# Kernel tuning notes

Measured on AMD Instinct MI355X. Metric: run time of the kernel, lower is better.

The kernel has to match this reference:

```python
import jax, jax.numpy as jnp
import numpy as np
from jax import lax

B, C, H, W, T = 1, 32, 256, 256, 10
Q = 0.2  # dropout prob; keep prob = 0.8


def conv2d(x, w, b=None, pad=0):
    out = lax.conv_general_dilated(x, w, (1, 1), [(pad, pad), (pad, pad)],
                                   dimension_numbers=('NCHW', 'OIHW', 'NCHW'))
    if b is not None:
        out = out + b[None, :, None, None]
    return out


def lrelu(v):
    return jnp.where(v > 0, v, 0.2 * v)


def setup_inputs() -> dict:
    key = jax.random.key(0)
    ks = iter(jax.random.split(key, 80))
    def rn(shape, s=0.05):
        return jax.random.normal(next(ks), shape, jnp.float32) * s
    d = {}
    d['F_1'] = jax.random.normal(next(ks), (B, C, H, W), jnp.float32)
    d['ms'] = jax.random.normal(next(ks), (B, 4, H, W), jnp.float32)
    d['pan'] = jax.random.normal(next(ks), (B, C, H, W), jnp.float32)
    d['masks_u'] = jax.random.uniform(next(ks), (T, 2 * C), jnp.float32)
    # UncertaintyEstimation params
    d['ue_conv_w'] = rn((2 * C, C, 3, 3)); d['ue_conv_b'] = rn((2 * C,), 0.01)
    d['ue_out_w'] = rn((4, 2 * C, 1, 1)); d['ue_out_b'] = rn((4,), 0.01)
    d['ue_aue_w'] = rn((4, 2 * C, 3, 3)); d['ue_aue_b'] = rn((4,), 0.01)
    # UAFM 1x1 convs
    d['conv1_w'] = rn((C, C, 1, 1)); d['conv1_b'] = rn((C,), 0.01)
    d['conv2_w'] = rn((C, C, 1, 1)); d['conv2_b'] = rn((C,), 0.01)
    # two UAConvs (condition_channels=4, channels_in=2C, channels_out=C, k=3)
    for i in (1, 2):
        d[f'spa{i}_w0'] = rn((9, 4, 3, 3)); d[f'spa{i}_b0'] = rn((9,), 0.01)
        d[f'spa{i}_w1'] = rn((9, 9, 1, 1)); d[f'spa{i}_b1'] = rn((9,), 0.01)
        d[f'spa{i}_w2'] = rn((9, 9, 1, 1)); d[f'spa{i}_b2'] = rn((9,), 0.01)
        d[f'spe{i}_w0'] = rn((2 * C, 4, 1, 1)); d[f'spe{i}_b0'] = rn((2 * C,), 0.01)
        d[f'spe{i}_w1'] = rn((2 * C, 2 * C, 1, 1)); d[f'spe{i}_b1'] = rn((2 * C,), 0.01)
        d[f'spe{i}_w2'] = rn((2 * C, 2 * C, 1, 1)); d[f'spe{i}_b2'] = rn((2 * C,), 0.01)
        d[f'ua{i}_w'] = rn((C, 2 * C, 3, 3))
    return d


def uaconv(x, U, sw0, sb0, sw1, sb1, sw2, sb2, pw0, pb0, pw1, pb1, pw2, pb2, Wk):
    # content-adaptive conv: per-pixel spatial (k*k) and spectral (n) attention
    b, n, h, w = x.shape
    a = jax.nn.relu(conv2d(U, sw0, sb0, 1))
    a = jax.nn.relu(conv2d(a, sw1, sb1, 0))
    spat = jax.nn.sigmoid(conv2d(a, sw2, sb2, 0))          # [B, 9, H, W]
    s = jax.nn.relu(conv2d(U, pw0, pb0, 0))
    s = jax.nn.relu(conv2d(s, pw1, pb1, 0))
    spec = jax.nn.sigmoid(conv2d(s, pw2, pb2, 0))          # [B, n, H, W]
    # unfold: patches channel order (c, kh, kw), matching F.unfold
    patches = lax.conv_general_dilated_patches(x, (3, 3), (1, 1), [(1, 1), (1, 1)])
    patches = patches.reshape(b, n, 9, h, w)               # [B, n, 9, H, W]
    rw = patches * spec[:, :, None] * spat[:, None]        # reweight
    Wr = Wk.reshape(Wk.shape[0], n, 9)                     # [m, n, 9]
    return jnp.einsum('bnkhw,mnk->bmhw', rw, Wr)           # fold(k=1) == reshape


def reference(F_1, ms, pan, masks_u,
              ue_conv_w, ue_conv_b, ue_out_w, ue_out_b, ue_aue_w, ue_aue_b,
              conv1_w, conv1_b, conv2_w, conv2_b,
              spa1_w0, spa1_b0, spa1_w1, spa1_b1, spa1_w2, spa1_b2,
              spe1_w0, spe1_b0, spe1_w1, spe1_b1, spe1_w2, spe1_b2, ua1_w,
              spa2_w0, spa2_b0, spa2_w1, spa2_b1, spa2_w2, spa2_b2,
              spe2_w0, spe2_b0, spe2_w1, spe2_b1, spe2_w2, spe2_b2, ua2_w):
    # --- UncertaintyEstimation ---
    x = conv2d(F_1, ue_conv_w, ue_conv_b, 1)               # [B, 2C, H, W]
    mask = (masks_u < (1.0 - Q)).astype(x.dtype)           # [T, 2C] Bernoulli(0.8)
    w4 = ue_out_w[:, :, 0, 0]                              # 1x1 conv as matmul
    # T masked passes, vectorized: xs [T, B, 4, H, W]
    xs = jnp.tanh(jnp.einsum('tc,oc,bchw->tbohw', mask, w4, x)
                  + ue_out_b[None, None, :, None, None]) + ms[None]
    EU = jnp.var(xs, axis=0, ddof=1)                       # unbiased over T
    mean = jnp.mean(xs, axis=0)
    AU = jax.nn.sigmoid(conv2d(x, ue_aue_w, ue_aue_b, 1))
    # --- UAFM ---
    y1 = uaconv(jnp.concatenate([F_1, pan], axis=1), EU,
                spa1_w0, spa1_b0, spa1_w1, spa1_b1, spa1_w2, spa1_b2,
                spe1_w0, spe1_b0, spe1_w1, spe1_b1, spe1_w2, spe1_b2, ua1_w)
    F_2 = lrelu(conv2d(y1, conv1_w, conv1_b, 0))
    y2 = uaconv(jnp.concatenate([F_1, F_2], axis=1), 1.0 - EU,
                spa2_w0, spa2_b0, spa2_w1, spa2_b1, spa2_w2, spa2_b2,
                spe2_w0, spe2_b0, spe2_w1, spe2_b1, spe2_w2, spe2_b2, ua2_w)
    F_out = lrelu(conv2d(y2, conv2_w, conv2_b, 0))
    return (AU, EU, mean, F_out)
```

## Files before the change

kernel.cpp:

```cpp
#include <hip/hip_runtime.h>
#include <hip/hip_bf16.h>
#include <math.h>
#include <string.h>

#define P 65536
#define HH 256
#define WW 256

typedef __attribute__((ext_vector_type(8))) short bf16x8;
typedef __attribute__((ext_vector_type(4))) float f32x4;

__device__ __forceinline__ float fast_sigmoid(float v) {
    return 1.f / (1.f + __expf(-v));
}
__device__ __forceinline__ float fast_tanh(float a) {
    a = fminf(fmaxf(a, -10.f), 10.f);
    float t = __expf(2.f * a);
    return (t - 1.f) / (t + 1.f);
}
__device__ __forceinline__ ushort f2bf(float f) {
    unsigned u = __float_as_uint(f);
    unsigned r = (u + 0x7fffu + ((u >> 16) & 1u)) >> 16;
    return (ushort)r;
}
__device__ __forceinline__ unsigned pack_bf2(float a, float b) {
    __hip_bfloat162 h = __float22bfloat162_rn(make_float2(a, b));
    unsigned u;
    memcpy(&u, &h, 4);
    return u;
}

__global__ __launch_bounds__(256) void setup_k(
        const float* __restrict__ F1, const float* __restrict__ pan,
        ushort* __restrict__ xbf, ushort* __restrict__ panbf,
        const float* __restrict__ ue_w, const float* __restrict__ aue_w,
        const float* __restrict__ ua1, const float* __restrict__ ua2,
        const float* __restrict__ s1w1, const float* __restrict__ s1w2,
        const float* __restrict__ s2w1, const float* __restrict__ s2w2,
        const float* __restrict__ cw1, const float* __restrict__ cw2,
        const float* __restrict__ masks_u, const float* __restrict__ w4,
        float* __restrict__ W, ushort* __restrict__ wub) {
    const int b = blockIdx.x;
    if (b < 512) {
        int idx = b * 256 + threadIdx.x;
        const float* src = (idx < P) ? F1 : pan;
        ushort* dst = (idx < P) ? xbf : panbf;
        int p = idx & (P - 1);
        unsigned pk[16];
        #pragma unroll
        for (int c = 0; c < 16; ++c) {
            float a = src[(2 * c) * P + p];
            float bb = src[(2 * c + 1) * P + p];
            pk[c] = (unsigned)f2bf(a) | ((unsigned)f2bf(bb) << 16);
        }
        uint4* d4 = (uint4*)(dst + (size_t)p * 32);
        #pragma unroll
        for (int q = 0; q < 4; ++q)
            d4[q] = make_uint4(pk[4 * q], pk[4 * q + 1], pk[4 * q + 2], pk[4 * q + 3]);
        return;
    }
    int i = (b - 512) * 256 + threadIdx.x;
    if (i < 2304) {
        int ci = i / 36, r = i % 36, k = r >> 2, co = r & 3;
        W[i] = aue_w[co * 576 + ci * 9 + k];
    } else if (i < 18688) {
    } else if (i < 21248) {
        int j = i - 18688;
        int t = j >> 8, o = (j >> 6) & 3, c = j & 63;
        W[i] = (masks_u[t * 64 + c] < 0.8f) ? w4[o * 64 + c] : 0.f;
    } else if (i < 39680) {
        int j = i - 21248;
        int ct = j / 4608, r1 = j % 4608;
        int kp = r1 / 512, r2 = r1 % 512;
        int n = r2 >> 5, ci = r2 & 31;
        wub[j] = f2bf(ue_w[(ct * 16 + n) * 288 + ci * 9 + kp]);
    } else if (i < 58112) {
        int j = i - 39680;
        int mo = j / 576, K = j % 576, k = K >> 6, n = K & 63;
        float s = 0.f;
        for (int m = 0; m < 32; ++m)
            s += cw1[mo * 32 + m] * ua1[m * 576 + n * 9 + k];
        wub[18432 + j] = f2bf(s);
    } else if (i < 76544) {
        int j = i - 58112;
        int mo = j / 576, K = j % 576, k = K >> 6, n = K & 63;
        float s = 0.f;
        for (int m = 0; m < 32; ++m)
            s += cw2[mo * 32 + m] * ua2[m * 576 + n * 9 + k];
        wub[36864 + j] = f2bf(s);
    } else if (i < 92928) {
        int j = i - 76544;
        int mat = j >> 12;
        int r = j & 4095;
        int ct = r >> 10, kk = (r >> 9) & 1, n = (r >> 5) & 15, c = r & 31;
        const float* src = (mat == 0) ? s1w1 : (mat == 1) ? s1w2
                         : (mat == 2) ? s2w1 : s2w2;
        wub[55296 + j] = f2bf(src[(ct * 16 + n) * 64 + kk * 32 + c]);
    }
}

__global__ __launch_bounds__(256) void conv_ue_mfma(
        const ushort* __restrict__ xbf, const ushort* __restrict__ wbfu,
        const float* __restrict__ bias, ushort* __restrict__ xnh) {
    __shared__ float tls[4][272];
    const int tid  = threadIdx.x;
    const int lane = tid & 63;
    const int wv   = __builtin_amdgcn_readfirstlane(tid >> 6);
    const int lrow = lane & 15;
    const int kg   = lane >> 4;

    bf16x8 zf;
    #pragma unroll
    for (int z = 0; z < 8; ++z) zf[z] = 0;

    bf16x8 Bf[9];
    const ushort* wb = wbfu + wv * 4608;
    #pragma unroll
    for (int kp = 0; kp < 9; ++kp)
        Bf[kp] = *(const bf16x8*)(wb + kp * 512 + lrow * 32 + kg * 8);

    const float bco = bias[wv * 16 + lrow];
    float* tw = tls[wv];

    for (int si = 0; si < 4; ++si) {
        const int s   = blockIdx.x * 4 + si;
        const int row = s >> 4;
        const int cb  = (s & 15) << 4;
        const int pb  = s << 4;
        f32x4 acc = {bco, bco, bco, bco};
        #pragma unroll
        for (int dh = -1; dh <= 1; ++dh) {
            if ((unsigned)(row + dh) >= 256u) continue;
            #pragma unroll
            for (int dw = -1; dw <= 1; ++dw) {
                const bool kill = (dw == -1 && cb == 0 && lrow == 0) ||
                                  (dw == 1 && cb == 240 && lrow == 15);
                const int apx = kill ? pb : (pb + dh * 256 + dw + lrow);
                bf16x8 Af = *(const bf16x8*)(xbf + (size_t)apx * 32 + kg * 8);
                if (kill) Af = zf;
                acc = __builtin_amdgcn_mfma_f32_16x16x32_bf16(
                          Af, Bf[(dh + 1) * 3 + (dw + 1)], acc, 0, 0, 0);
            }
        }
        #pragma unroll
        for (int j = 0; j < 4; ++j)
            tw[(kg * 4 + j) * 17 + lrow] = acc[j];
        asm volatile("s_waitcnt lgkmcnt(0)" ::: "memory");
        {
            const float* rp = tw + lrow * 17;
            unsigned o[8];
            #pragma unroll
            for (int q = 0; q < 8; ++q)
                o[q] = pack_bf2(rp[2 * q], rp[2 * q + 1]);
            ushort* dst = xnh + (size_t)(pb + lrow) * 64 + wv * 16;
            *(uint4*)dst       = make_uint4(o[0], o[1], o[2], o[3]);
            *(uint4*)(dst + 8) = make_uint4(o[4], o[5], o[6], o[7]);
        }
        asm volatile("s_waitcnt lgkmcnt(0)" ::: "memory");
    }
}

__global__ __launch_bounds__(256) void head_k(
        const ushort* __restrict__ xnh, const float* __restrict__ aue_wt,
        const float* __restrict__ aue_b, const float* __restrict__ mw,
        const float* __restrict__ b4, const float* __restrict__ msin,
        float* __restrict__ AU, float* __restrict__ EU, float* __restrict__ MEAN) {
    __shared__ float cs[64][65];
    __shared__ float pr[4][4][64];
    const int tid = threadIdx.x;
    const int pxg = tid & 63;
    const int g   = __builtin_amdgcn_readfirstlane(tid >> 6);
    const int p   = blockIdx.x * 64 + pxg;
    const int h = p >> 8, x0 = p & 255;
    const int cib = g * 16;

    float pa[4] = {0.f, 0.f, 0.f, 0.f};
    float cv[16];
    #pragma unroll
    for (int k = 0; k < 9; ++k) {
        const int dh = k / 3 - 1, dw = k % 3 - 1;
        if ((unsigned)(h + dh) >= 256u) continue;
        const bool kill = (dw == -1 && x0 == 0) || (dw == 1 && x0 == 255);
        const int pxe = kill ? p : (p + dh * 256 + dw);
        const ushort* sp = xnh + (size_t)pxe * 64 + cib;
        uint4 ra = *(const uint4*)sp;
        uint4 rb = *(const uint4*)(sp + 8);
        unsigned rr[8] = {ra.x, ra.y, ra.z, ra.w, rb.x, rb.y, rb.z, rb.w};
        if (kill) {
            #pragma unroll
            for (int q = 0; q < 8; ++q) rr[q] = 0;
        }
        float f[16];
        #pragma unroll
        for (int q = 0; q < 8; ++q) {
            f[2 * q]     = __uint_as_float(rr[q] << 16);
            f[2 * q + 1] = __uint_as_float(rr[q] & 0xffff0000u);
        }
        if (k == 4) {
            #pragma unroll
            for (int ci = 0; ci < 16; ++ci) cv[ci] = f[ci];
        }
        #pragma unroll
        for (int ci = 0; ci < 16; ++ci) {
            const float* wp = aue_wt + (cib + ci) * 36 + k * 4;
            #pragma unroll
            for (int co = 0; co < 4; ++co)
                pa[co] = fmaf(f[ci], wp[co], pa[co]);
        }
    }
    #pragma unroll
    for (int co = 0; co < 4; ++co) pr[co][g][pxg] = pa[co];
    #pragma unroll
    for (int ci = 0; ci < 16; ++ci) cs[pxg][cib + ci] = cv[ci];
    __syncthreads();

    {
        float s = aue_b[g] + pr[g][0][pxg] + pr[g][1][pxg]
                           + pr[g][2][pxg] + pr[g][3][pxg];
        AU[g * P + p] = fast_sigmoid(s);
    }

    float xv[64];
    #pragma unroll
    for (int c = 0; c < 64; ++c) xv[c] = cs[pxg][c];
    float msv = msin[g * P + p];
    float bo  = b4[g];
    float vals[10];
    float s = 0.f;
    #pragma unroll
    for (int t = 0; t < 10; ++t) {
        float a = bo;
        const float* mwp = mw + t * 256 + g * 64;
        #pragma unroll
        for (int c = 0; c < 64; ++c) a = fmaf(mwp[c], xv[c], a);
        float v = fast_tanh(a) + msv;
        vals[t] = v;
        s += v;
    }
    float m = s * 0.1f;
    MEAN[g * P + p] = m;
    float var = 0.f;
    #pragma unroll
    for (int t = 0; t < 10; ++t) { float d = vals[t] - m; var = fmaf(d, d, var); }
    EU[g * P + p] = var * (1.0f / 9.0f);
}

template<int OUTMODE>
__global__ __launch_bounds__(256) void ua_fused_k(
        const float* __restrict__ U, int flip,
        const float* __restrict__ aw0, const float* __restrict__ ab0,
        const float* __restrict__ aw1, const float* __restrict__ ab1,
        const float* __restrict__ aw2, const float* __restrict__ ab2,
        const float* __restrict__ pw0, const float* __restrict__ pb0,
        const float* __restrict__ pb1, const float* __restrict__ pb2,
        const ushort* __restrict__ wspe,
        const ushort* __restrict__ xa, const ushort* __restrict__ xb,
        const ushort* __restrict__ w2bf, const float* __restrict__ cb,
        float* __restrict__ outf, ushort* __restrict__ outh) {
    __shared__ __align__(16) ushort ping[64 * 72];
    __shared__ __align__(16) ushort pong[64 * 72];
    __shared__ float spat_l[9][64];
    const int tid = threadIdx.x;
    const int pxg = tid & 63;
    const int g   = __builtin_amdgcn_readfirstlane(tid >> 6);
    const int cib = g * 16;
    const int p   = blockIdx.x * 64 + pxg;
    const int h = p >> 8, x0 = p & 255;
    const int lane = tid & 63;
    const int lrow = lane & 15;
    const int kg   = lane >> 4;

    bf16x8 Wf[2][4][2];
    #pragma unroll
    for (int ly = 0; ly < 2; ++ly)
        #pragma unroll
        for (int ct = 0; ct < 4; ++ct)
            #pragma unroll
            for (int kk = 0; kk < 2; ++kk)
                Wf[ly][ct][kk] = *(const bf16x8*)(wspe + ly * 4096 +
                                     ct * 1024 + kk * 512 + lrow * 32 + kg * 8);

    {
        float u[4];
        #pragma unroll
        for (int ci = 0; ci < 4; ++ci) {
            float v = U[ci * P + p];
            u[ci] = flip ? 1.f - v : v;
        }
        unsigned* prow = (unsigned*)ping + (pxg * 72 + cib) / 2;
        #pragma unroll
        for (int cl = 0; cl < 8; ++cl) {
            int c0 = cib + 2 * cl, c1 = c0 + 1;
            float s0 = pb0[c0], s1 = pb0[c1];
            #pragma unroll
            for (int k = 0; k < 4; ++k) {
                s0 = fmaf(u[k], pw0[c0 * 4 + k], s0);
                s1 = fmaf(u[k], pw0[c1 * 4 + k], s1);
            }
            prow[cl] = pack_bf2(fmaxf(s0, 0.f), fmaxf(s1, 0.f));
        }
    }
    __syncthreads();

    #pragma unroll
    for (int ct = 0; ct < 4; ++ct) {
        f32x4 a = {0.f, 0.f, 0.f, 0.f};
        #pragma unroll
        for (int kk = 0; kk < 2; ++kk) {
            bf16x8 A = *(const bf16x8*)&ping[(g * 16 + lrow) * 72 + kk * 32 + kg * 8];
            a = __builtin_amdgcn_mfma_f32_16x16x32_bf16(A, Wf[0][ct][kk], a, 0, 0, 0);
        }
        float b = pb1[ct * 16 + lrow];
        #pragma unroll
        for (int j = 0; j < 4; ++j)
            pong[(g * 16 + kg * 4 + j) * 72 + ct * 16 + lrow] = f2bf(fmaxf(a[j] + b, 0.f));
    }
    asm volatile("s_waitcnt lgkmcnt(0)" ::: "memory");
    #pragma unroll
    for (int ct = 0; ct < 4; ++ct) {
        f32x4 a = {0.f, 0.f, 0.f, 0.f};
        #pragma unroll
        for (int kk = 0; kk < 2; ++kk) {
            bf16x8 A = *(const bf16x8*)&pong[(g * 16 + lrow) * 72 + kk * 32 + kg * 8];
            a = __builtin_amdgcn_mfma_f32_16x16x32_bf16(A, Wf[1][ct][kk], a, 0, 0, 0);
        }
        float b = pb2[ct * 16 + lrow];
        #pragma unroll
        for (int j = 0; j < 4; ++j)
            ping[(g * 16 + kg * 4 + j) * 72 + ct * 16 + lrow] =
                f2bf(fast_sigmoid(a[j] + b));
    }

    {
        float uh[4][9];
        #pragma unroll
        for (int ci = 0; ci < 4; ++ci) {
            const float* up = U + ci * P;
            #pragma unroll
            for (int kh = 0; kh < 3; ++kh) {
                int hh = h + kh - 1;
                bool hok = (unsigned)hh < 256u;
                #pragma unroll
                for (int kw = 0; kw < 3; ++kw) {
                    int wx = x0 + kw - 1;
                    bool ok = hok && (unsigned)wx < 256u;
                    float v = ok ? up[hh * WW + wx] : 0.f;
                    if (flip && ok) v = 1.f - v;
                    uh[ci][kh * 3 + kw] = v;
                }
            }
        }
        float a1[9];
        #pragma unroll
        for (int co = 0; co < 9; ++co) {
            float s = ab0[co];
            #pragma unroll
            for (int ci = 0; ci < 4; ++ci)
                #pragma unroll
                for (int k = 0; k < 9; ++k)
                    s = fmaf(uh[ci][k], aw0[co * 36 + ci * 9 + k], s);
            a1[co] = fmaxf(s, 0.f);
        }
        float a2[9];
        #pragma unroll
        for (int co = 0; co < 9; ++co) {
            float s = ab1[co];
            #pragma unroll
            for (int ci = 0; ci < 9; ++ci) s = fmaf(a1[ci], aw1[co * 9 + ci], s);
            a2[co] = fmaxf(s, 0.f);
        }
        #pragma unroll
        for (int cq = 0; cq < 3; ++cq) {
            const int co = g + cq * 4;
            if (co < 9) {
                float s = ab2[co];
                #pragma unroll
                for (int ci = 0; ci < 9; ++ci) s = fmaf(a2[ci], aw2[co * 9 + ci], s);
                spat_l[co][pxg] = fast_sigmoid(s);
            }
        }
    }
    __syncthreads();

    const int wv   = g;
    const int s    = blockIdx.x * 4 + wv;
    const int row  = s >> 4;
    const int c16  = s & 15;
    const int pb   = s << 4;
    const int px   = pb + lrow;
    const int pxl  = wv * 16 + lrow;

    float sl[8], sh[8];
    {
        const unsigned* sp = (const unsigned*)&ping[pxl * 72 + kg * 8];
        #pragma unroll
        for (int q = 0; q < 4; ++q) {
            unsigned uu = sp[q];
            sl[2 * q]     = __uint_as_float(uu << 16);
            sl[2 * q + 1] = __uint_as_float(uu & 0xffff0000u);
        }
        const unsigned* sp2 = (const unsigned*)&ping[pxl * 72 + 32 + kg * 8];
        #pragma unroll
        for (int q = 0; q < 4; ++q) {
            unsigned uu = sp2[q];
            sh[2 * q]     = __uint_as_float(uu << 16);
            sh[2 * q + 1] = __uint_as_float(uu & 0xffff0000u);
        }
    }
    const ushort* b0p = w2bf + lrow * 576 + kg * 8;
    const ushort* b1p = w2bf + (16 + lrow) * 576 + kg * 8;

    f32x4 acc0 = {0.f, 0.f, 0.f, 0.f};
    f32x4 acc1 = {0.f, 0.f, 0.f, 0.f};

    #pragma unroll
    for (int k = 0; k < 9; ++k) {
        const int dh = k / 3 - 1, dw = k % 3 - 1;
        if ((unsigned)(row + dh) >= 256u) continue;
        const bool kill = (dw == -1 && c16 == 0 && lrow == 0) ||
                          (dw == 1 && c16 == 15 && lrow == 15);
        float stk = spat_l[k][pxl];
        if (kill) stk = 0.f;
        const int pxe = kill ? px : (px + dh * 256 + dw);
        #pragma unroll
        for (int par = 0; par < 2; ++par) {
            const ushort* src = (par == 0) ? (xa + (size_t)pxe * 32 + kg * 8)
                                           : (xb + (size_t)pxe * 32 + kg * 8);
            uint4 raw = *(const uint4*)src;
            const float* ss = par ? sh : sl;
            unsigned rr[4] = {raw.x, raw.y, raw.z, raw.w};
            union { unsigned u[4]; bf16x8 v; } af;
            #pragma unroll
            for (int q = 0; q < 4; ++q) {
                float e0 = __uint_as_float(rr[q] << 16)          * (ss[2 * q] * stk);
                float e1 = __uint_as_float(rr[q] & 0xffff0000u)  * (ss[2 * q + 1] * stk);
                af.u[q] = pack_bf2(e0, e1);
            }
            const int ki = k * 2 + par;
            bf16x8 bf0 = *(const bf16x8*)(b0p + ki * 32);
            bf16x8 bf1 = *(const bf16x8*)(b1p + ki * 32);
            acc0 = __builtin_amdgcn_mfma_f32_16x16x32_bf16(af.v, bf0, acc0, 0, 0, 0);
            acc1 = __builtin_amdgcn_mfma_f32_16x16x32_bf16(af.v, bf1, acc1, 0, 0, 0);
        }
    }

    const float cb0 = cb[lrow], cb1 = cb[16 + lrow];
    float* tw = (float*)pong + wv * 560;
    #pragma unroll
    for (int j = 0; j < 4; ++j) {
        float y0 = acc0[j] + cb0; y0 = y0 > 0.f ? y0 : 0.2f * y0;
        float y1 = acc1[j] + cb1; y1 = y1 > 0.f ? y1 : 0.2f * y1;
        tw[(kg * 4 + j) * 35 + lrow] = y0;
        tw[(kg * 4 + j) * 35 + 16 + lrow] = y1;
    }
    asm volatile("s_waitcnt lgkmcnt(0)" ::: "memory");
    if constexpr (OUTMODE == 0) {
        const float* rp = tw + lrow * 35 + kg * 8;
        unsigned o[4];
        #pragma unroll
        for (int q = 0; q < 4; ++q)
            o[q] = pack_bf2(rp[2 * q], rp[2 * q + 1]);
        *(uint4*)(outh + (size_t)(pb + lrow) * 32 + kg * 8) =
            make_uint4(o[0], o[1], o[2], o[3]);
    } else {
        #pragma unroll
        for (int it = 0; it < 8; ++it) {
            const int mo = kg * 8 + it;
            outf[mo * P + pb + lrow] = tw[lrow * 35 + mo];
        }
    }
    asm volatile("s_waitcnt lgkmcnt(0)" ::: "memory");
}

extern "C" void kernel_launch(void* const* d_in, const int* in_sizes, int n_in,
                              void* d_out, int out_size, void* d_ws, size_t ws_size,
                              hipStream_t stream) {
    const float* F1        = (const float*)d_in[0];
    const float* ms        = (const float*)d_in[1];
    const float* pan       = (const float*)d_in[2];
    const float* masks_u   = (const float*)d_in[3];
    const float* ue_conv_w = (const float*)d_in[4];
    const float* ue_conv_b = (const float*)d_in[5];
    const float* ue_out_w  = (const float*)d_in[6];
    const float* ue_out_b  = (const float*)d_in[7];
    const float* ue_aue_w  = (const float*)d_in[8];
    const float* ue_aue_b  = (const float*)d_in[9];
    const float* conv1_w   = (const float*)d_in[10];
    const float* conv1_b   = (const float*)d_in[11];
    const float* conv2_w   = (const float*)d_in[12];
    const float* conv2_b   = (const float*)d_in[13];
    const float* spa1_w0 = (const float*)d_in[14];
    const float* spa1_b0 = (const float*)d_in[15];
    const float* spa1_w1 = (const float*)d_in[16];
    const float* spa1_b1 = (const float*)d_in[17];
    const float* spa1_w2 = (const float*)d_in[18];
    const float* spa1_b2 = (const float*)d_in[19];
    const float* spe1_w0 = (const float*)d_in[20];
    const float* spe1_b0 = (const float*)d_in[21];
    const float* spe1_w1 = (const float*)d_in[22];
    const float* spe1_b1 = (const float*)d_in[23];
    const float* spe1_w2 = (const float*)d_in[24];
    const float* spe1_b2 = (const float*)d_in[25];
    const float* ua1_w   = (const float*)d_in[26];
    const float* spa2_w0 = (const float*)d_in[27];
    const float* spa2_b0 = (const float*)d_in[28];
    const float* spa2_w1 = (const float*)d_in[29];
    const float* spa2_b1 = (const float*)d_in[30];
    const float* spa2_w2 = (const float*)d_in[31];
    const float* spa2_b2 = (const float*)d_in[32];
    const float* spe2_w0 = (const float*)d_in[33];
    const float* spe2_b0 = (const float*)d_in[34];
    const float* spe2_w1 = (const float*)d_in[35];
    const float* spe2_b1 = (const float*)d_in[36];
    const float* spe2_w2 = (const float*)d_in[37];
    const float* spe2_b2 = (const float*)d_in[38];
    const float* ua2_w   = (const float*)d_in[39];

    float* out  = (float*)d_out;
    float* AU   = out;
    float* EU   = out + 4 * P;
    float* MEAN = out + 8 * P;
    float* FOUT = out + 12 * P;

    float* ws    = (float*)d_ws;
    ushort* xbf   = (ushort*)ws;
    ushort* panbf = (ushort*)(ws + 16 * P);
    ushort* xnh   = (ushort*)(ws + 32 * P);
    ushort* f2nh  = (ushort*)(ws + 64 * P);
    float* W     = ws + 80 * P;
    float* aue_wt = W;
    float* mw     = W + 18688;
    ushort* wub   = (ushort*)(W + 21248);
    ushort* wbfu  = wub;
    ushort* w2bf1 = wub + 18432;
    ushort* w2bf2 = wub + 36864;
    ushort* wspe1 = wub + 55296;
    ushort* wspe2 = wub + 63488;

    dim3 blk(256);

    setup_k<<<dim3(875), blk, 0, stream>>>(F1, pan, xbf, panbf,
                                           ue_conv_w, ue_aue_w, ua1_w, ua2_w,
                                           spe1_w1, spe1_w2, spe2_w1, spe2_w2,
                                           conv1_w, conv2_w, masks_u, ue_out_w, W, wub);

    conv_ue_mfma<<<dim3(1024), blk, 0, stream>>>(xbf, wbfu, ue_conv_b, xnh);
    head_k<<<dim3(1024), blk, 0, stream>>>(xnh, aue_wt, ue_aue_b, mw, ue_out_b, ms,
                                           AU, EU, MEAN);

    ua_fused_k<0><<<dim3(1024), blk, 0, stream>>>(
        EU, 0,
        spa1_w0, spa1_b0, spa1_w1, spa1_b1, spa1_w2, spa1_b2,
        spe1_w0, spe1_b0, spe1_b1, spe1_b2, wspe1,
        xbf, panbf, w2bf1, conv1_b, nullptr, f2nh);

    ua_fused_k<1><<<dim3(1024), blk, 0, stream>>>(
        EU, 1,
        spa2_w0, spa2_b0, spa2_w1, spa2_b1, spa2_w2, spa2_b2,
        spe2_w0, spe2_b0, spe2_b1, spe2_b2, wspe2,
        xbf, f2nh, w2bf2, conv2_b, FOUT, nullptr);
}
```

Measured before the change: 113.7 us.

## Move head AU conv and masked-dropout projections onto bf16 MFMA

The head kernel's 3x3 AU conv and the ten masked 1x1 output projections were scalar FP32 FMAs with LDS staging and a block barrier. They now run as 16x16x32 bf16 MFMAs over weights packed and padded to bf16 in the setup kernel. Mean and variance are computed from sums and sums of squares combined with cross-lane shuffles. The uaconv kernel also loads its 3x3 uncertainty neighbourhood earlier and reuses the centre tap. This trades FP32 accuracy for bf16 weights and a one-pass variance formula, which is less numerically stable.

```diff
diff --git a/kernel.cpp b/kernel.cpp
--- a/kernel.cpp
+++ b/kernel.cpp
@@ -39,7 +39,7 @@
         const float* __restrict__ s2w1, const float* __restrict__ s2w2,
         const float* __restrict__ cw1, const float* __restrict__ cw2,
         const float* __restrict__ masks_u, const float* __restrict__ w4,
-        float* __restrict__ W, ushort* __restrict__ wub) {
+        ushort* __restrict__ wub) {
     const int b = blockIdx.x;
     if (b < 512) {
         int idx = b * 256 + threadIdx.x;
@@ -60,42 +60,45 @@
         return;
     }
     int i = (b - 512) * 256 + threadIdx.x;
-    if (i < 2304) {
-        int ci = i / 36, r = i % 36, k = r >> 2, co = r & 3;
-        W[i] = aue_w[co * 576 + ci * 9 + k];
-    } else if (i < 18688) {
-    } else if (i < 21248) {
-        int j = i - 18688;
-        int t = j >> 8, o = (j >> 6) & 3, c = j & 63;
-        W[i] = (masks_u[t * 64 + c] < 0.8f) ? w4[o * 64 + c] : 0.f;
-    } else if (i < 39680) {
-        int j = i - 21248;
-        int ct = j / 4608, r1 = j % 4608;
+    if (i < 18432) {
+        int ct = i / 4608, r1 = i % 4608;
         int kp = r1 / 512, r2 = r1 % 512;
         int n = r2 >> 5, ci = r2 & 31;
-        wub[j] = f2bf(ue_w[(ct * 16 + n) * 288 + ci * 9 + kp]);
-    } else if (i < 58112) {
-        int j = i - 39680;
+        wub[i] = f2bf(ue_w[(ct * 16 + n) * 288 + ci * 9 + kp]);
+    } else if (i < 36864) {
+        int j = i - 18432;
         int mo = j / 576, K = j % 576, k = K >> 6, n = K & 63;
         float s = 0.f;
         for (int m = 0; m < 32; ++m)
             s += cw1[mo * 32 + m] * ua1[m * 576 + n * 9 + k];
-        wub[18432 + j] = f2bf(s);
-    } else if (i < 76544) {
-        int j = i - 58112;
+        wub[i] = f2bf(s);
+    } else if (i < 55296) {
+        int j = i - 36864;
         int mo = j / 576, K = j % 576, k = K >> 6, n = K & 63;
         float s = 0.f;
         for (int m = 0; m < 32; ++m)
             s += cw2[mo * 32 + m] * ua2[m * 576 + n * 9 + k];
-        wub[36864 + j] = f2bf(s);
-    } else if (i < 92928) {
-        int j = i - 76544;
+        wub[i] = f2bf(s);
+    } else if (i < 71680) {
+        int j = i - 55296;
         int mat = j >> 12;
         int r = j & 4095;
         int ct = r >> 10, kk = (r >> 9) & 1, n = (r >> 5) & 15, c = r & 31;
         const float* src = (mat == 0) ? s1w1 : (mat == 1) ? s1w2
                          : (mat == 2) ? s2w1 : s2w2;
-        wub[55296 + j] = f2bf(src[(ct * 16 + n) * 64 + kk * 32 + c]);
+        wub[i] = f2bf(src[(ct * 16 + n) * 64 + kk * 32 + c]);
+    } else if (i < 74752) {
+        int j = i - 71680;
+        int r = j >> 6, c = j & 63;
+        int t = r >> 2, o = r & 3;
+        float v = (t < 10 && masks_u[t * 64 + c] < 0.8f) ? w4[o * 64 + c] : 0.f;
+        wub[i] = f2bf(v);
+    } else if (i < 83968) {
+        int j = i - 74752;
+        int r = j / 576, rem = j % 576;
+        int tap = rem >> 6, ci = rem & 63;
+        float v = (r < 4) ? aue_w[r * 576 + ci * 9 + tap] : 0.f;
+        wub[i] = f2bf(v);
     }
 }
 
@@ -161,88 +164,90 @@
 }
 
 __global__ __launch_bounds__(256) void head_k(
-        const ushort* __restrict__ xnh, const float* __restrict__ aue_wt,
-        const float* __restrict__ aue_b, const float* __restrict__ mw,
+        const ushort* __restrict__ xnh, const ushort* __restrict__ awbf,
+        const ushort* __restrict__ mwbf, const float* __restrict__ aue_b,
         const float* __restrict__ b4, const float* __restrict__ msin,
         float* __restrict__ AU, float* __restrict__ EU, float* __restrict__ MEAN) {
-    __shared__ float cs[64][65];
-    __shared__ float pr[4][4][64];
-    const int tid = threadIdx.x;
-    const int pxg = tid & 63;
-    const int g   = __builtin_amdgcn_readfirstlane(tid >> 6);
-    const int p   = blockIdx.x * 64 + pxg;
-    const int h = p >> 8, x0 = p & 255;
-    const int cib = g * 16;
-
-    float pa[4] = {0.f, 0.f, 0.f, 0.f};
-    float cv[16];
-    #pragma unroll
-    for (int k = 0; k < 9; ++k) {
-        const int dh = k / 3 - 1, dw = k % 3 - 1;
-        if ((unsigned)(h + dh) >= 256u) continue;
+    const int tid  = threadIdx.x;
+    const int lane = tid & 63;
+    const int wv   = __builtin_amdgcn_readfirstlane(tid >> 6);
+    const int lrow = lane & 15;
+    const int kg   = lane >> 4;
+    const int pb   = blockIdx.x * 64 + wv * 16;
+    const int px   = pb + lrow;
+    const int row  = pb >> 8;
+    const int x0   = px & 255;
+
+    bf16x8 zf;
+    #pragma unroll
+    for (int z = 0; z < 8; ++z) zf[z] = 0;
+
+    f32x4 aacc = {0.f, 0.f, 0.f, 0.f};
+    bf16x8 ctr[2];
+    ctr[0] = zf; ctr[1] = zf;
+
+    #pragma unroll
+    for (int tap = 0; tap < 9; ++tap) {
+        const int dh = tap / 3 - 1, dw = tap % 3 - 1;
+        if ((unsigned)(row + dh) >= 256u) continue;
         const bool kill = (dw == -1 && x0 == 0) || (dw == 1 && x0 == 255);
-        const int pxe = kill ? p : (p + dh * 256 + dw);
-        const ushort* sp = xnh + (size_t)pxe * 64 + cib;
-        uint4 ra = *(const uint4*)sp;
-        uint4 rb = *(const uint4*)(sp + 8);
-        unsigned rr[8] = {ra.x, ra.y, ra.z, ra.w, rb.x, rb.y, rb.z, rb.w};
-        if (kill) {
-            #pragma unroll
-            for (int q = 0; q < 8; ++q) rr[q] = 0;
-        }
-        float f[16];
-        #pragma unroll
-        for (int q = 0; q < 8; ++q) {
-            f[2 * q]     = __uint_as_float(rr[q] << 16);
-            f[2 * q + 1] = __uint_as_float(rr[q] & 0xffff0000u);
-        }
-        if (k == 4) {
-            #pragma unroll
-            for (int ci = 0; ci < 16; ++ci) cv[ci] = f[ci];
-        }
-        #pragma unroll
-        for (int ci = 0; ci < 16; ++ci) {
-            const float* wp = aue_wt + (cib + ci) * 36 + k * 4;
-            #pragma unroll
-            for (int co = 0; co < 4; ++co)
-                pa[co] = fmaf(f[ci], wp[co], pa[co]);
-        }
-    }
-    #pragma unroll
-    for (int co = 0; co < 4; ++co) pr[co][g][pxg] = pa[co];
-    #pragma unroll
-    for (int ci = 0; ci < 16; ++ci) cs[pxg][cib + ci] = cv[ci];
-    __syncthreads();
-
-    {
-        float s = aue_b[g] + pr[g][0][pxg] + pr[g][1][pxg]
-                           + pr[g][2][pxg] + pr[g][3][pxg];
-        AU[g * P + p] = fast_sigmoid(s);
-    }
-
-    float xv[64];
-    #pragma unroll
-    for (int c = 0; c < 64; ++c) xv[c] = cs[pxg][c];
-    float msv = msin[g * P + p];
-    float bo  = b4[g];
-    float vals[10];
-    float s = 0.f;
-    #pragma unroll
-    for (int t = 0; t < 10; ++t) {
-        float a = bo;
-        const float* mwp = mw + t * 256 + g * 64;
-        #pragma unroll
-        for (int c = 0; c < 64; ++c) a = fmaf(mwp[c], xv[c], a);
-        float v = fast_tanh(a) + msv;
-        vals[t] = v;
-        s += v;
-    }
-    float m = s * 0.1f;
-    MEAN[g * P + p] = m;
-    float var = 0.f;
-    #pragma unroll
-    for (int t = 0; t < 10; ++t) { float d = vals[t] - m; var = fmaf(d, d, var); }
-    EU[g * P + p] = var * (1.0f / 9.0f);
+        const int pxe = kill ? px : (px + dh * 256 + dw);
+        #pragma unroll
+        for (int half = 0; half < 2; ++half) {
+            bf16x8 B = *(const bf16x8*)(xnh + (size_t)pxe * 64 + half * 32 + kg * 8);
+            if (kill) B = zf;
+            if (tap == 4) ctr[half] = B;
+            bf16x8 A = *(const bf16x8*)(awbf + lrow * 576 + (tap * 2 + half) * 32 + kg * 8);
+            aacc = __builtin_amdgcn_mfma_f32_16x16x32_bf16(A, B, aacc, 0, 0, 0);
+        }
+    }
+    if (kg == 0) {
+        #pragma unroll
+        for (int j = 0; j < 4; ++j)
+            AU[j * P + px] = fast_sigmoid(aacc[j] + aue_b[j]);
+    }
+
+    f32x4 xacc[3];
+    const f32x4 binit = {b4[0], b4[1], b4[2], b4[3]};
+    xacc[0] = binit; xacc[1] = binit; xacc[2] = binit;
+    #pragma unroll
+    for (int rt = 0; rt < 3; ++rt) {
+        #pragma unroll
+        for (int half = 0; half < 2; ++half) {
+            bf16x8 A = *(const bf16x8*)(mwbf + (rt * 16 + lrow) * 64 + half * 32 + kg * 8);
+            xacc[rt] = __builtin_amdgcn_mfma_f32_16x16x32_bf16(A, ctr[half], xacc[rt], 0, 0, 0);
+        }
+    }
+    float msv[4];
+    #pragma unroll
+    for (int j = 0; j < 4; ++j) msv[j] = msin[j * P + px];
+    float S[4] = {0.f, 0.f, 0.f, 0.f};
+    float Q[4] = {0.f, 0.f, 0.f, 0.f};
+    #pragma unroll
+    for (int rt = 0; rt < 3; ++rt) {
+        const int t = rt * 4 + kg;
+        const bool valid = t < 10;
+        #pragma unroll
+        for (int j = 0; j < 4; ++j) {
+            float v = fast_tanh(xacc[rt][j]) + msv[j];
+            if (valid) { S[j] += v; Q[j] = fmaf(v, v, Q[j]); }
+        }
+    }
+    #pragma unroll
+    for (int j = 0; j < 4; ++j) {
+        S[j] += __shfl_xor(S[j], 16);
+        S[j] += __shfl_xor(S[j], 32);
+        Q[j] += __shfl_xor(Q[j], 16);
+        Q[j] += __shfl_xor(Q[j], 32);
+    }
+    if (kg == 0) {
+        #pragma unroll
+        for (int j = 0; j < 4; ++j) {
+            float m = S[j] * 0.1f;
+            MEAN[j * P + px] = m;
+            EU[j * P + px] = (Q[j] - S[j] * S[j] * 0.1f) * (1.0f / 9.0f);
+        }
+    }
 }
 
 template<int OUTMODE>
@@ -270,6 +275,25 @@
     const int lrow = lane & 15;
     const int kg   = lane >> 4;
 
+    float uh[4][9];
+    #pragma unroll
+    for (int ci = 0; ci < 4; ++ci) {
+        const float* up = U + ci * P;
+        #pragma unroll
+        for (int kh = 0; kh < 3; ++kh) {
+            int hh = h + kh - 1;
+            bool hok = (unsigned)hh < 256u;
+            #pragma unroll
+            for (int kw = 0; kw < 3; ++kw) {
+                int wx = x0 + kw - 1;
+                bool ok = hok && (unsigned)wx < 256u;
+                float v = ok ? up[hh * WW + wx] : 0.f;
+                if (flip && ok) v = 1.f - v;
+                uh[ci][kh * 3 + kw] = v;
+            }
+        }
+    }
+
     bf16x8 Wf[2][4][2];
     #pragma unroll
     for (int ly = 0; ly < 2; ++ly)
@@ -283,10 +307,7 @@
     {
         float u[4];
         #pragma unroll
-        for (int ci = 0; ci < 4; ++ci) {
-            float v = U[ci * P + p];
-            u[ci] = flip ? 1.f - v : v;
-        }
+        for (int ci = 0; ci < 4; ++ci) u[ci] = uh[ci][4];
         unsigned* prow = (unsigned*)ping + (pxg * 72 + cib) / 2;
         #pragma unroll
         for (int cl = 0; cl < 8; ++cl) {
@@ -332,24 +353,6 @@
     }
 
     {
-        float uh[4][9];
-        #pragma unroll
-        for (int ci = 0; ci < 4; ++ci) {
-            const float* up = U + ci * P;
-            #pragma unroll
-            for (int kh = 0; kh < 3; ++kh) {
-                int hh = h + kh - 1;
-                bool hok = (unsigned)hh < 256u;
-                #pragma unroll
-                for (int kw = 0; kw < 3; ++kw) {
-                    int wx = x0 + kw - 1;
-                    bool ok = hok && (unsigned)wx < 256u;
-                    float v = ok ? up[hh * WW + wx] : 0.f;
-                    if (flip && ok) v = 1.f - v;
-                    uh[ci][kh * 3 + kw] = v;
-                }
-            }
-        }
         float a1[9];
         #pragma unroll
         for (int co = 0; co < 9; ++co) {
@@ -527,25 +530,24 @@
     ushort* panbf = (ushort*)(ws + 16 * P);
     ushort* xnh   = (ushort*)(ws + 32 * P);
     ushort* f2nh  = (ushort*)(ws + 64 * P);
-    float* W     = ws + 80 * P;
-    float* aue_wt = W;
-    float* mw     = W + 18688;
-    ushort* wub   = (ushort*)(W + 21248);
+    ushort* wub   = (ushort*)(ws + 80 * P);
     ushort* wbfu  = wub;
     ushort* w2bf1 = wub + 18432;
     ushort* w2bf2 = wub + 36864;
     ushort* wspe1 = wub + 55296;
     ushort* wspe2 = wub + 63488;
+    ushort* mwbf  = wub + 71680;
+    ushort* awbf  = wub + 74752;
 
     dim3 blk(256);
 
-    setup_k<<<dim3(875), blk, 0, stream>>>(F1, pan, xbf, panbf,
+    setup_k<<<dim3(840), blk, 0, stream>>>(F1, pan, xbf, panbf,
                                            ue_conv_w, ue_aue_w, ua1_w, ua2_w,
                                            spe1_w1, spe1_w2, spe2_w1, spe2_w2,
-                                           conv1_w, conv2_w, masks_u, ue_out_w, W, wub);
+                                           conv1_w, conv2_w, masks_u, ue_out_w, wub);
 
     conv_ue_mfma<<<dim3(1024), blk, 0, stream>>>(xbf, wbfu, ue_conv_b, xnh);
-    head_k<<<dim3(1024), blk, 0, stream>>>(xnh, aue_wt, ue_aue_b, mw, ue_out_b, ms,
+    head_k<<<dim3(1024), blk, 0, stream>>>(xnh, awbf, mwbf, ue_aue_b, ue_out_b, ms,
                                            AU, EU, MEAN);
 
     ua_fused_k<0><<<dim3(1024), blk, 0, stream>>>(
```

New measurement: 123.4 us. 1.09x slower.
